# Kernel optimization log

Measured on AMD Instinct MI355X. Metric: run time of the kernel, lower is better.

Reference implementation:

```python
import jax, jax.numpy as jnp
import numpy as np

N_NODES = 50000
N_EDGES = 800000
IN_F, OUT_F = 128, 128
NUM_HEADS, QUERY_DIM = 3, 8


def setup_inputs() -> dict:
    key = jax.random.key(0)
    ks = jax.random.split(key, 8)
    scale = 1.0 / np.sqrt(IN_F)
    return {
        "x": jax.random.normal(ks[0], (N_NODES, IN_F), dtype=jnp.float32),
        "adj": jax.random.randint(ks[1], (2, N_EDGES), 0, N_NODES, dtype=jnp.int64),
        "Wq": jax.random.normal(ks[2], (QUERY_DIM * NUM_HEADS, IN_F), dtype=jnp.float32) * scale,
        "bq": jax.random.normal(ks[3], (QUERY_DIM * NUM_HEADS,), dtype=jnp.float32) * 0.01,
        "aw": jax.random.normal(ks[4], (NUM_HEADS, 2 * QUERY_DIM * NUM_HEADS), dtype=jnp.float32) * 0.1,
        "ab": jax.random.normal(ks[5], (NUM_HEADS,), dtype=jnp.float32) * 0.01,
        "lw": jax.random.normal(ks[6], (OUT_F, IN_F), dtype=jnp.float32) * scale,
        "lb": jax.random.normal(ks[7], (OUT_F,), dtype=jnp.float32) * 0.01,
    }


def reference(x, adj, Wq, bq, aw, ab, lw, lb):
    n = x.shape[0]
    s, r = adj[0], adj[1]
    # per-node query features: [N, H*Q]
    attr = x @ Wq.T + bq
    # per-edge attention logits from concat(sender, receiver): [E, H]
    e = jnp.concatenate((attr[s], attr[r]), axis=1) @ aw.T + ab
    # segment softmax over incoming edges of each receiver
    seg_max = jax.ops.segment_max(e, r, num_segments=n)  # [N, H]
    e = jnp.exp(e - jax.lax.stop_gradient(seg_max)[r])
    denom = jax.ops.segment_sum(e, r, num_segments=n)  # [N, H]
    alpha = e / jnp.maximum(denom[r], 1e-16)  # [E, H]
    # node value projection and attention-weighted aggregation
    h = x @ lw.T + lb  # [N, OUT_F]
    msg = h[s] * alpha.mean(axis=1, keepdims=True)  # [E, OUT_F]
    out = jax.ops.segment_sum(msg, r, num_segments=n)  # [N, OUT_F]
    return jax.nn.silu(out)
```

## Files before the change

kernel.cpp:

```cpp
#include <hip/hip_runtime.h>
#include <hip/hip_fp16.h>
#include <math.h>

#define N_NODES 50000
#define N_EDGES 800000
#define IN_F 128
#define OUT_F 128
#define NH 3
#define SCAN_NB ((N_NODES + 255) / 256)
#define NODE_NB ((N_NODES + 31) / 32)
#define NBH 32
#define EPB (N_EDGES / NBH)
#define QNODES (N_NODES / 4)
#define CQ_BLOCKS (NBH * 4)

typedef __attribute__((ext_vector_type(8))) _Float16 f16x8;
typedef __attribute__((ext_vector_type(4))) float f32x4;

__global__ __launch_bounds__(256) void weights_kernel(
    const float* __restrict__ Wq, const float* __restrict__ bq,
    const float* __restrict__ aw, const float* __restrict__ ab,
    const float* __restrict__ lw,
    _Float16* __restrict__ w2h, float* __restrict__ b2,
    _Float16* __restrict__ lwh)
{
    int t = blockIdx.x * 256 + threadIdx.x;
    if (t < 16 * 128) {
        int prow = t >> 7;
        int i    = t & 127;
        int r = -1;
        if (prow < 3) r = prow;
        else if (prow >= 4 && prow < 7) r = prow - 1;
        if (r < 0) {
            w2h[prow * 128 + i] = (_Float16)0.0f;
        } else {
            int hh  = (r < 3) ? r : r - 3;
            int off = (r < 3) ? 0 : 24;
            const float* awr = aw + hh * 48 + off;
            float acc = 0.0f;
            #pragma unroll
            for (int q = 0; q < 24; q++) acc += awr[q] * Wq[q * 128 + i];
            w2h[prow * 128 + i] = (_Float16)acc;
            if (i == 0) {
                float b = 0.0f;
                #pragma unroll
                for (int q = 0; q < 24; q++) b += awr[q] * bq[q];
                if (r >= 3) b += ab[hh];
                b2[r] = b;
            }
        }
    }
    int u = t - 16 * 128;
    if (u >= 0 && u < 128 * 128) lwh[u] = (_Float16)lw[u];
}

__global__ __launch_bounds__(256) void node_count_kernel(
    const float* __restrict__ x, const _Float16* __restrict__ lwh,
    const float* __restrict__ lb, const _Float16* __restrict__ w2h,
    const float* __restrict__ b2, const int* __restrict__ adj,
    __half* __restrict__ h, float* __restrict__ as4, float* __restrict__ ar4,
    unsigned int* __restrict__ hist, unsigned short* __restrict__ rank)
{
    __shared__ __align__(16) unsigned int shmem[QNODES / 2];

    if (blockIdx.x < CQ_BLOCKS) {
        unsigned int* cnt = shmem;
        for (int i = threadIdx.x; i < QNODES / 2; i += 256) cnt[i] = 0;
        __syncthreads();
        const int c = blockIdx.x >> 2, q = blockIdx.x & 3;
        const int nlo = q * QNODES;
        const int e0 = c * EPB, e1 = e0 + EPB;
        for (int base = e0 + threadIdx.x; base < e1; base += 8 * 256) {
            int rs[8];
            #pragma unroll
            for (int u = 0; u < 8; u++) {
                int e = base + u * 256;
                rs[u] = (e < e1) ? adj[N_EDGES + e] : -1;
            }
            #pragma unroll
            for (int u = 0; u < 8; u++) {
                int e = base + u * 256;
                int lr = rs[u] - nlo;
                if ((unsigned)lr < (unsigned)QNODES) {
                    int sh = (lr & 1) * 16;
                    unsigned int old = atomicAdd(&cnt[lr >> 1], 1u << sh);
                    rank[e] = (unsigned short)(old >> sh);
                }
            }
        }
        __syncthreads();
        unsigned int* hb = hist + (size_t)c * (N_NODES / 2) + q * (QNODES / 2);
        for (int i = threadIdx.x; i < QNODES / 2; i += 256)
            hb[i] = cnt[i];
        return;
    }

    unsigned char* xs = (unsigned char*)shmem;
    const int tx = threadIdx.x;
    const int nb = (blockIdx.x - CQ_BLOCKS) * 32;

    #pragma unroll
    for (int it = 0; it < 2; it++) {
        int cc = it * 256 + tx;
        int node = cc >> 4, kc = cc & 15;
        int gn = nb + node;
        f16x8 v;
        if (gn < N_NODES) {
            const float4* xr = (const float4*)(x + (size_t)gn * 128 + kc * 8);
            float4 p = xr[0], qq = xr[1];
            v[0] = (_Float16)p.x;  v[1] = (_Float16)p.y;
            v[2] = (_Float16)p.z;  v[3] = (_Float16)p.w;
            v[4] = (_Float16)qq.x; v[5] = (_Float16)qq.y;
            v[6] = (_Float16)qq.z; v[7] = (_Float16)qq.w;
        } else {
            #pragma unroll
            for (int e = 0; e < 8; e++) v[e] = (_Float16)0.0f;
        }
        int byte = node * 256 + ((kc * 16) ^ ((node & 7) << 4));
        *(f16x8*)(xs + byte) = v;
    }
    __syncthreads();

    const int wave = tx >> 6, lane = tx & 63;
    const int l15 = lane & 15, lg = lane >> 4;

    f16x8 afr[2][4];
    #pragma unroll
    for (int m = 0; m < 2; m++) {
        int out = wave * 32 + m * 16 + l15;
        const f16x8* ar8 = (const f16x8*)(lwh + (size_t)out * 128);
        #pragma unroll
        for (int kk = 0; kk < 4; kk++)
            afr[m][kk] = ar8[kk * 4 + lg];
    }
    f16x8 a6[4];
    {
        const f16x8* w8 = (const f16x8*)(w2h + (size_t)l15 * 128);
        #pragma unroll
        for (int kk = 0; kk < 4; kk++) a6[kk] = w8[kk * 4 + lg];
    }

    f32x4 acc[2][2], acc6[2];
    #pragma unroll
    for (int m = 0; m < 2; m++)
        #pragma unroll
        for (int n = 0; n < 2; n++)
            acc[m][n] = (f32x4){0.f, 0.f, 0.f, 0.f};
    #pragma unroll
    for (int n = 0; n < 2; n++) acc6[n] = (f32x4){0.f, 0.f, 0.f, 0.f};

    #pragma unroll
    for (int kk = 0; kk < 4; kk++) {
        f16x8 bfr[2];
        #pragma unroll
        for (int n = 0; n < 2; n++) {
            int node = n * 16 + l15;
            int byte = node * 256 + ((kk * 64 + lg * 16) ^ ((node & 7) << 4));
            bfr[n] = *(const f16x8*)(xs + byte);
        }
        #pragma unroll
        for (int m = 0; m < 2; m++)
            #pragma unroll
            for (int n = 0; n < 2; n++)
                acc[m][n] = __builtin_amdgcn_mfma_f32_16x16x32_f16(
                    afr[m][kk], bfr[n], acc[m][n], 0, 0, 0);
        if (wave == 0) {
            #pragma unroll
            for (int n = 0; n < 2; n++)
                acc6[n] = __builtin_amdgcn_mfma_f32_16x16x32_f16(
                    a6[kk], bfr[n], acc6[n], 0, 0, 0);
        }
    }

    #pragma unroll
    for (int n = 0; n < 2; n++) {
        int gn = nb + n * 16 + l15;
        if (gn >= N_NODES) continue;
        #pragma unroll
        for (int m = 0; m < 2; m++) {
            int outb = wave * 32 + m * 16 + lg * 4;
            float4 lbv = *(const float4*)&lb[outb];
            __half2 p0 = __floats2half2_rn(acc[m][n].x + lbv.x, acc[m][n].y + lbv.y);
            __half2 p1 = __floats2half2_rn(acc[m][n].z + lbv.z, acc[m][n].w + lbv.w);
            int2 st;
            st.x = *(int*)&p0;
            st.y = *(int*)&p1;
            *(int2*)&h[(size_t)gn * 128 + outb] = st;
        }
    }

    if (wave == 0 && lg < 2) {
        float b0, bx, by;
        if (lg == 0) { b0 = b2[0]; bx = b2[1]; by = b2[2]; }
        else         { b0 = b2[3]; bx = b2[4]; by = b2[5]; }
        #pragma unroll
        for (int n = 0; n < 2; n++) {
            int gn = nb + n * 16 + l15;
            if (gn >= N_NODES) continue;
            float4 v = make_float4(acc6[n].x + b0, acc6[n].y + bx,
                                   acc6[n].z + by, 0.0f);
            if (lg == 0) *(float4*)&as4[(size_t)gn * 4] = v;
            else         *(float4*)&ar4[(size_t)gn * 4] = v;
        }
    }
}

__global__ __launch_bounds__(256) void scan_kernel(
    const unsigned int* __restrict__ hist, int* __restrict__ start,
    unsigned short* __restrict__ offs16,
    int* __restrict__ psum, int* __restrict__ poffs, int* __restrict__ sync)
{
    const int t = threadIdx.x, b = blockIdx.x;
    const int i = b * 256 + t;
    const int w = i >> 1, sh = (i & 1) * 16;
    int tot = 0;
    if (i < N_NODES) {
        for (int c = 0; c < NBH; c++)
            tot += (hist[(size_t)c * (N_NODES / 2) + w] >> sh) & 0xffff;
    }
    __shared__ int shm[256];
    shm[t] = tot;
    __syncthreads();
    #pragma unroll
    for (int off = 1; off < 256; off <<= 1) {
        int u = (t >= off) ? shm[t - off] : 0;
        __syncthreads();
        shm[t] += u;
        __syncthreads();
    }
    const int incl = shm[t];
    if (t == 255)
        __hip_atomic_store(&psum[b], incl, __ATOMIC_RELAXED,
                           __HIP_MEMORY_SCOPE_AGENT);
    __syncthreads();
    if (t == 0)
        __hip_atomic_fetch_add(&sync[0], 1, __ATOMIC_RELEASE,
                               __HIP_MEMORY_SCOPE_AGENT);

    if (b == 0) {
        if (t == 0)
            while (__hip_atomic_load(&sync[0], __ATOMIC_ACQUIRE,
                                     __HIP_MEMORY_SCOPE_AGENT) < SCAN_NB) {}
        __syncthreads();
        int pv = (t < SCAN_NB)
               ? __hip_atomic_load(&psum[t], __ATOMIC_RELAXED,
                                   __HIP_MEMORY_SCOPE_AGENT)
               : 0;
        shm[t] = pv;
        __syncthreads();
        #pragma unroll
        for (int off = 1; off < 256; off <<= 1) {
            int u = (t >= off) ? shm[t - off] : 0;
            __syncthreads();
            shm[t] += u;
            __syncthreads();
        }
        if (t < SCAN_NB)
            __hip_atomic_store(&poffs[t], shm[t] - pv, __ATOMIC_RELAXED,
                               __HIP_MEMORY_SCOPE_AGENT);
        __syncthreads();
        if (t == 0)
            __hip_atomic_store(&sync[1], 1, __ATOMIC_RELEASE,
                               __HIP_MEMORY_SCOPE_AGENT);
    }

    if (t == 0)
        while (__hip_atomic_load(&sync[1], __ATOMIC_ACQUIRE,
                                 __HIP_MEMORY_SCOPE_AGENT) == 0) {}
    __syncthreads();
    const int base = __hip_atomic_load(&poffs[b], __ATOMIC_RELAXED,
                                       __HIP_MEMORY_SCOPE_AGENT);
    if (i < N_NODES) {
        start[i] = base + incl - tot;
        int acc = 0;
        for (int c = 0; c < NBH; c++) {
            offs16[(size_t)c * N_NODES + i] = (unsigned short)acc;
            acc += (hist[(size_t)c * (N_NODES / 2) + w] >> sh) & 0xffff;
        }
    }
    if (i == N_NODES - 1) start[N_NODES] = base + incl;
}

__global__ __launch_bounds__(256) void fill_kernel(
    const int* __restrict__ adj, const int* __restrict__ start,
    const unsigned short* __restrict__ offs16,
    const unsigned short* __restrict__ rank,
    unsigned short* __restrict__ srcs)
{
    int e = blockIdx.x * 512 + threadIdx.x;
    #pragma unroll
    for (int u = 0; u < 2; u++, e += 256) {
        if (e < N_EDGES) {
            int r = adj[N_EDGES + e];
            int cb = e / EPB;
            int pos = start[r] + (int)offs16[(size_t)cb * N_NODES + r]
                    + (int)rank[e];
            srcs[pos] = (unsigned short)adj[e];
        }
    }
}

__global__ __launch_bounds__(256) void agg_kernel(
    const int* __restrict__ start, const unsigned short* __restrict__ srcs,
    const float4* __restrict__ as4, const float* __restrict__ ar4,
    const __half* __restrict__ h, float* __restrict__ out)
{
    const int wave = threadIdx.x >> 6;
    const int lane = threadIdx.x & 63;
    const int n = blockIdx.x * 4 + wave;
    if (n >= N_NODES) return;
    const int s0 = start[n], s1 = start[n + 1];
    const int deg = s1 - s0;

    __shared__ float sh_c[4][64];
    __shared__ int   sh_s[4][64];

    const float4 cr = *(const float4*)&ar4[(size_t)n * 4];
    const int quar = lane >> 4, l15 = lane & 15;
    const int4* hq = (const int4*)h;
    float a0 = 0.f, a1 = 0.f, a2 = 0.f, a3 = 0.f;
    float a4 = 0.f, a5 = 0.f, a6 = 0.f, a7 = 0.f;

    if (deg <= 64) {
        float e0 = 0.f, e1 = 0.f, e2 = 0.f;
        int s = 0;
        if (lane < deg) {
            s = srcs[s0 + lane];
            float4 a = as4[s];
            e0 = __expf(a.x + cr.x);
            e1 = __expf(a.y + cr.y);
            e2 = __expf(a.z + cr.z);
        }
        float p0 = e0, p1 = e1, p2 = e2;
        #pragma unroll
        for (int off = 32; off >= 1; off >>= 1) {
            p0 += __shfl_xor(p0, off);
            p1 += __shfl_xor(p1, off);
            p2 += __shfl_xor(p2, off);
        }
        const float i0 = (1.0f / 3.0f) / fmaxf(p0, 1e-30f);
        const float i1 = (1.0f / 3.0f) / fmaxf(p1, 1e-30f);
        const float i2 = (1.0f / 3.0f) / fmaxf(p2, 1e-30f);
        if (lane < deg) {
            sh_s[wave][lane] = s;
            sh_c[wave][lane] = e0 * i0 + e1 * i1 + e2 * i2;
        } else if (lane < deg + 3) {
            sh_s[wave][lane] = 0;
            sh_c[wave][lane] = 0.0f;
        }
        #pragma unroll 2
        for (int j = 0; j < deg; j += 4) {
            int jj = j + quar;
            float c = sh_c[wave][jj];
            int sj = sh_s[wave][jj];
            int4 hv = hq[(size_t)sj * 16 + l15];
            float2 f0 = __half22float2(*(const __half2*)&hv.x);
            float2 f1 = __half22float2(*(const __half2*)&hv.y);
            float2 f2 = __half22float2(*(const __half2*)&hv.z);
            float2 f3 = __half22float2(*(const __half2*)&hv.w);
            a0 = fmaf(f0.x, c, a0); a1 = fmaf(f0.y, c, a1);
            a2 = fmaf(f1.x, c, a2); a3 = fmaf(f1.y, c, a3);
            a4 = fmaf(f2.x, c, a4); a5 = fmaf(f2.y, c, a5);
            a6 = fmaf(f3.x, c, a6); a7 = fmaf(f3.y, c, a7);
        }
    } else {
        float p0 = 0.f, p1 = 0.f, p2 = 0.f;
        for (int k = s0 + lane; k < s1; k += 64) {
            float4 a = as4[srcs[k]];
            p0 += __expf(a.x + cr.x);
            p1 += __expf(a.y + cr.y);
            p2 += __expf(a.z + cr.z);
        }
        #pragma unroll
        for (int off = 32; off >= 1; off >>= 1) {
            p0 += __shfl_xor(p0, off);
            p1 += __shfl_xor(p1, off);
            p2 += __shfl_xor(p2, off);
        }
        const float i0 = (1.0f / 3.0f) / fmaxf(p0, 1e-30f);
        const float i1 = (1.0f / 3.0f) / fmaxf(p1, 1e-30f);
        const float i2 = (1.0f / 3.0f) / fmaxf(p2, 1e-30f);

        for (int cb = s0; cb < s1; cb += 64) {
            int cnt = min(64, s1 - cb);
            if (lane < cnt) {
                int s = srcs[cb + lane];
                float4 a = as4[s];
                sh_s[wave][lane] = s;
                sh_c[wave][lane] = __expf(a.x + cr.x) * i0
                                 + __expf(a.y + cr.y) * i1
                                 + __expf(a.z + cr.z) * i2;
            } else if (lane < cnt + 3) {
                sh_s[wave][lane] = 0;
                sh_c[wave][lane] = 0.0f;
            }
            #pragma unroll 2
            for (int j = 0; j < cnt; j += 4) {
                int jj = j + quar;
                float c = sh_c[wave][jj];
                int sj = sh_s[wave][jj];
                int4 hv = hq[(size_t)sj * 16 + l15];
                float2 f0 = __half22float2(*(const __half2*)&hv.x);
                float2 f1 = __half22float2(*(const __half2*)&hv.y);
                float2 f2 = __half22float2(*(const __half2*)&hv.z);
                float2 f3 = __half22float2(*(const __half2*)&hv.w);
                a0 = fmaf(f0.x, c, a0); a1 = fmaf(f0.y, c, a1);
                a2 = fmaf(f1.x, c, a2); a3 = fmaf(f1.y, c, a3);
                a4 = fmaf(f2.x, c, a4); a5 = fmaf(f2.y, c, a5);
                a6 = fmaf(f3.x, c, a6); a7 = fmaf(f3.y, c, a7);
            }
        }
    }

    a0 += __shfl_xor(a0, 16); a0 += __shfl_xor(a0, 32);
    a1 += __shfl_xor(a1, 16); a1 += __shfl_xor(a1, 32);
    a2 += __shfl_xor(a2, 16); a2 += __shfl_xor(a2, 32);
    a3 += __shfl_xor(a3, 16); a3 += __shfl_xor(a3, 32);
    a4 += __shfl_xor(a4, 16); a4 += __shfl_xor(a4, 32);
    a5 += __shfl_xor(a5, 16); a5 += __shfl_xor(a5, 32);
    a6 += __shfl_xor(a6, 16); a6 += __shfl_xor(a6, 32);
    a7 += __shfl_xor(a7, 16); a7 += __shfl_xor(a7, 32);

    if (quar == 0) {
        float4 o0, o1;
        o0.x = a0 / (1.0f + __expf(-a0));
        o0.y = a1 / (1.0f + __expf(-a1));
        o0.z = a2 / (1.0f + __expf(-a2));
        o0.w = a3 / (1.0f + __expf(-a3));
        o1.x = a4 / (1.0f + __expf(-a4));
        o1.y = a5 / (1.0f + __expf(-a5));
        o1.z = a6 / (1.0f + __expf(-a6));
        o1.w = a7 / (1.0f + __expf(-a7));
        *(float4*)&out[(size_t)n * 128 + l15 * 8] = o0;
        *(float4*)&out[(size_t)n * 128 + l15 * 8 + 4] = o1;
    }
}

extern "C" void kernel_launch(void* const* d_in, const int* in_sizes, int n_in,
                              void* d_out, int out_size, void* d_ws, size_t ws_size,
                              hipStream_t stream)
{
    const float* x  = (const float*)d_in[0];
    const int*   adj= (const int*)  d_in[1];
    const float* Wq = (const float*)d_in[2];
    const float* bq = (const float*)d_in[3];
    const float* aw = (const float*)d_in[4];
    const float* ab = (const float*)d_in[5];
    const float* lw = (const float*)d_in[6];
    const float* lb = (const float*)d_in[7];
    float* out = (float*)d_out;

    _Float16* w2h = (_Float16*)d_ws;
    float* b2     = (float*)(w2h + 2048);
    _Float16* lwh = (_Float16*)(b2 + 8);
    float* as4    = (float*)(lwh + 16384);
    float* ar4    = as4 + (size_t)N_NODES * 4;
    __half* h     = (__half*)(ar4 + (size_t)N_NODES * 4);
    int* start    = (int*)(h + (size_t)N_NODES * 128);
    int* sync     = start + (N_NODES + 1);
    unsigned int* hist = (unsigned int*)(sync + 8);
    unsigned short* offs16 = (unsigned short*)(hist + (size_t)NBH * (N_NODES / 2));
    unsigned short* rank   = offs16 + (size_t)NBH * N_NODES;
    unsigned short* srcs   = rank + N_EDGES;
    int* psum     = (int*)(srcs + N_EDGES);
    int* poffs    = psum + 256;

    hipMemsetAsync(sync, 0, 8 * sizeof(int), stream);

    weights_kernel<<<72, 256, 0, stream>>>(Wq, bq, aw, ab, lw, w2h, b2, lwh);

    node_count_kernel<<<CQ_BLOCKS + NODE_NB, 256, 0, stream>>>(
        x, lwh, lb, w2h, b2, adj, h, as4, ar4, hist, rank);

    scan_kernel<<<SCAN_NB, 256, 0, stream>>>(hist, start, offs16,
                                             psum, poffs, sync);

    fill_kernel<<<(N_EDGES + 511) / 512, 256, 0, stream>>>(
        adj, start, offs16, rank, srcs);

    agg_kernel<<<(N_NODES + 3) / 4, 256, 0, stream>>>(
        start, srcs, (const float4*)as4, ar4, h, out);
}
```

Measured before the change: 121.4 us.

## Fuse scan and fill via grid barrier, use fma_mix in aggregation

Merges the scan and fill kernels into one kernel, using a software grid barrier on a sync counter so each block scatters edges into CSR after all offsets are known. The memset of the sync flags moves into the weights kernel, which removes one memset and one kernel launch. The aggregation inner loop swaps the half-to-float conversions plus fmaf for inline v_fma_mix_f32 asm and raises the unroll factor from 2 to 4. The grid barrier needs all 196 scan blocks to be co-resident, and the fill now runs with far fewer threads per edge.

```diff
diff --git a/kernel.cpp b/kernel.cpp
--- a/kernel.cpp
+++ b/kernel.cpp
@@ -17,14 +17,22 @@
 typedef __attribute__((ext_vector_type(8))) _Float16 f16x8;
 typedef __attribute__((ext_vector_type(4))) float f32x4;
 
+#define FMA_MIX_LO(acc, w, c) \
+    asm("v_fma_mix_f32 %0, %1, %2, %0 op_sel:[0,0,0] op_sel_hi:[1,0,0]" \
+        : "+v"(acc) : "v"(w), "v"(c))
+#define FMA_MIX_HI(acc, w, c) \
+    asm("v_fma_mix_f32 %0, %1, %2, %0 op_sel:[1,0,0] op_sel_hi:[1,0,0]" \
+        : "+v"(acc) : "v"(w), "v"(c))
+
 __global__ __launch_bounds__(256) void weights_kernel(
     const float* __restrict__ Wq, const float* __restrict__ bq,
     const float* __restrict__ aw, const float* __restrict__ ab,
     const float* __restrict__ lw,
     _Float16* __restrict__ w2h, float* __restrict__ b2,
-    _Float16* __restrict__ lwh)
+    _Float16* __restrict__ lwh, int* __restrict__ sync)
 {
     int t = blockIdx.x * 256 + threadIdx.x;
+    if (blockIdx.x == 0 && threadIdx.x < 8) sync[threadIdx.x] = 0;
     if (t < 16 * 128) {
         int prow = t >> 7;
         int i    = t & 127;
@@ -205,10 +213,12 @@
     }
 }
 
-__global__ __launch_bounds__(256) void scan_kernel(
+__global__ __launch_bounds__(256) void scan_fill_kernel(
     const unsigned int* __restrict__ hist, int* __restrict__ start,
     unsigned short* __restrict__ offs16,
-    int* __restrict__ psum, int* __restrict__ poffs, int* __restrict__ sync)
+    int* __restrict__ psum, int* __restrict__ poffs, int* __restrict__ sync,
+    const int* __restrict__ adj, const unsigned short* __restrict__ rank,
+    unsigned short* __restrict__ srcs)
 {
     const int t = threadIdx.x, b = blockIdx.x;
     const int i = b * 256 + t;
@@ -279,24 +289,21 @@
         }
     }
     if (i == N_NODES - 1) start[N_NODES] = base + incl;
-}
-
-__global__ __launch_bounds__(256) void fill_kernel(
-    const int* __restrict__ adj, const int* __restrict__ start,
-    const unsigned short* __restrict__ offs16,
-    const unsigned short* __restrict__ rank,
-    unsigned short* __restrict__ srcs)
-{
-    int e = blockIdx.x * 512 + threadIdx.x;
-    #pragma unroll
-    for (int u = 0; u < 2; u++, e += 256) {
-        if (e < N_EDGES) {
-            int r = adj[N_EDGES + e];
-            int cb = e / EPB;
-            int pos = start[r] + (int)offs16[(size_t)cb * N_NODES + r]
-                    + (int)rank[e];
-            srcs[pos] = (unsigned short)adj[e];
-        }
+
+    __syncthreads();
+    if (t == 0) {
+        __hip_atomic_fetch_add(&sync[2], 1, __ATOMIC_RELEASE,
+                               __HIP_MEMORY_SCOPE_AGENT);
+        while (__hip_atomic_load(&sync[2], __ATOMIC_ACQUIRE,
+                                 __HIP_MEMORY_SCOPE_AGENT) < SCAN_NB) {}
+    }
+    __syncthreads();
+    for (int e = b * 256 + t; e < N_EDGES; e += SCAN_NB * 256) {
+        int r = adj[N_EDGES + e];
+        int cb = e / EPB;
+        int pos = start[r] + (int)offs16[(size_t)cb * N_NODES + r]
+                + (int)rank[e];
+        srcs[pos] = (unsigned short)adj[e];
     }
 }
 
@@ -348,20 +355,16 @@
             sh_s[wave][lane] = 0;
             sh_c[wave][lane] = 0.0f;
         }
-        #pragma unroll 2
+        #pragma unroll 4
         for (int j = 0; j < deg; j += 4) {
             int jj = j + quar;
             float c = sh_c[wave][jj];
             int sj = sh_s[wave][jj];
             int4 hv = hq[(size_t)sj * 16 + l15];
-            float2 f0 = __half22float2(*(const __half2*)&hv.x);
-            float2 f1 = __half22float2(*(const __half2*)&hv.y);
-            float2 f2 = __half22float2(*(const __half2*)&hv.z);
-            float2 f3 = __half22float2(*(const __half2*)&hv.w);
-            a0 = fmaf(f0.x, c, a0); a1 = fmaf(f0.y, c, a1);
-            a2 = fmaf(f1.x, c, a2); a3 = fmaf(f1.y, c, a3);
-            a4 = fmaf(f2.x, c, a4); a5 = fmaf(f2.y, c, a5);
-            a6 = fmaf(f3.x, c, a6); a7 = fmaf(f3.y, c, a7);
+            FMA_MIX_LO(a0, hv.x, c); FMA_MIX_HI(a1, hv.x, c);
+            FMA_MIX_LO(a2, hv.y, c); FMA_MIX_HI(a3, hv.y, c);
+            FMA_MIX_LO(a4, hv.z, c); FMA_MIX_HI(a5, hv.z, c);
+            FMA_MIX_LO(a6, hv.w, c); FMA_MIX_HI(a7, hv.w, c);
         }
     } else {
         float p0 = 0.f, p1 = 0.f, p2 = 0.f;
@@ -394,20 +397,16 @@
                 sh_s[wave][lane] = 0;
                 sh_c[wave][lane] = 0.0f;
             }
-            #pragma unroll 2
+            #pragma unroll 4
             for (int j = 0; j < cnt; j += 4) {
                 int jj = j + quar;
                 float c = sh_c[wave][jj];
                 int sj = sh_s[wave][jj];
                 int4 hv = hq[(size_t)sj * 16 + l15];
-                float2 f0 = __half22float2(*(const __half2*)&hv.x);
-                float2 f1 = __half22float2(*(const __half2*)&hv.y);
-                float2 f2 = __half22float2(*(const __half2*)&hv.z);
-                float2 f3 = __half22float2(*(const __half2*)&hv.w);
-                a0 = fmaf(f0.x, c, a0); a1 = fmaf(f0.y, c, a1);
-                a2 = fmaf(f1.x, c, a2); a3 = fmaf(f1.y, c, a3);
-                a4 = fmaf(f2.x, c, a4); a5 = fmaf(f2.y, c, a5);
-                a6 = fmaf(f3.x, c, a6); a7 = fmaf(f3.y, c, a7);
+                FMA_MIX_LO(a0, hv.x, c); FMA_MIX_HI(a1, hv.x, c);
+                FMA_MIX_LO(a2, hv.y, c); FMA_MIX_HI(a3, hv.y, c);
+                FMA_MIX_LO(a4, hv.z, c); FMA_MIX_HI(a5, hv.z, c);
+                FMA_MIX_LO(a6, hv.w, c); FMA_MIX_HI(a7, hv.w, c);
             }
         }
     }
@@ -465,18 +464,15 @@
     int* psum     = (int*)(srcs + N_EDGES);
     int* poffs    = psum + 256;
 
-    hipMemsetAsync(sync, 0, 8 * sizeof(int), stream);
-
-    weights_kernel<<<72, 256, 0, stream>>>(Wq, bq, aw, ab, lw, w2h, b2, lwh);
+    weights_kernel<<<72, 256, 0, stream>>>(Wq, bq, aw, ab, lw, w2h, b2, lwh,
+                                           sync);
 
     node_count_kernel<<<CQ_BLOCKS + NODE_NB, 256, 0, stream>>>(
         x, lwh, lb, w2h, b2, adj, h, as4, ar4, hist, rank);
 
-    scan_kernel<<<SCAN_NB, 256, 0, stream>>>(hist, start, offs16,
-                                             psum, poffs, sync);
-
-    fill_kernel<<<(N_EDGES + 511) / 512, 256, 0, stream>>>(
-        adj, start, offs16, rank, srcs);
+    scan_fill_kernel<<<SCAN_NB, 256, 0, stream>>>(hist, start, offs16,
+                                                  psum, poffs, sync,
+                                                  adj, rank, srcs);
 
     agg_kernel<<<(N_NODES + 3) / 4, 256, 0, stream>>>(
         start, srcs, (const float4*)as4, ar4, h, out);
```

Result: no change. 123.1 us (+1.4%).
